# Optimization experiments

Hardware: AMD Instinct MI355X
Metric: run time of the kernel (lower is better)

The kernel has to match this reference:

```python
import jax, jax.numpy as jnp
import numpy as np

B, T, V, NH, HD = 2, 64, 32000, 32, 32  # head_dim == n_head required by the original einsum
C = NH * HD

def setup_inputs() -> dict:
    key = jax.random.key(0)
    k0, k1, k2 = jax.random.split(key, 3)
    return {
        "x": jax.random.normal(k0, (B, T, C), jnp.float32),
        "W_ffn": jax.random.normal(k1, (HD, HD), jnp.float32) / np.sqrt(HD),
        "b_ffn": jnp.zeros((HD,), jnp.float32),
        "temps": jnp.ones((NH,), jnp.float32),
        "vocab_emb": jax.random.normal(k2, (V, C), jnp.float32) * 0.02,
    }

def reference(x, W_ffn, b_ffn, temps, vocab_emb):
    b, t, c = x.shape
    nh = temps.shape[0]
    hd = c // nh
    v = vocab_emb.shape[0]
    # per-head channel FFN: Linear(head_dim, head_dim) with bias -> x @ W^T + b
    xc = x.reshape(b * t, nh, hd)
    ffn = jnp.einsum('bnh,dh->bnd', xc, W_ffn) + b_ffn  # (BT, nh, hd)
    # vocab channels: (nh, V, hd)
    vocab_ch = vocab_emb.reshape(v, nh, hd).transpose(1, 0, 2)
    # Original torch einsum 'bnh,hvd->bnv' contracts ffn's head_dim axis with
    # vocab_ch's n_head axis (equal sizes) AND sums over d. Mathematically this
    # equals contracting against vocab_sum[h, v] = sum_d vocab_ch[h, v, d].
    vocab_sum = vocab_ch.sum(-1)  # (nh==hd, V)
    logits = jnp.einsum('bnh,hv->bnv', ffn, vocab_sum)  # (BT, nh, V)
    temps_c = jnp.clip(temps, 0.1)[None, :, None]
    weights = jax.nn.softmax(logits / temps_c, axis=-1)
    # Original 'bnv,hvd->bnh' likewise sums d: out[b,n,h] = sum_v w[b,n,v]*vocab_sum[h,v]
    out = jnp.einsum('bnv,hv->bnh', weights, vocab_sum)  # (BT, nh, hd)
    return out.reshape(b, t, c)
```

## Files before the change

### kernel.cpp

```cpp
#include <hip/hip_runtime.h>
#include <hip/hip_bf16.h>

#define NV      32000
#define MROWS   4096
#define NSLICE  16
#define PART_STRIDE 1056

typedef __attribute__((ext_vector_type(8))) short short8;
typedef __attribute__((ext_vector_type(16))) float f32x16;
typedef __attribute__((ext_vector_type(4))) float f32x4;

#define OFF_VSB  0
#define OFF_VSTB 2048000
#define OFF_FB   4096000
#define OFF_PART 4358144

#define NVS_BLOCKS 1000
#define NF_BLOCKS  512

static __device__ __forceinline__ unsigned pkbf(float lo, float hi) {
    union { __hip_bfloat162 h; unsigned u; } cv;
    cv.h.x = __float2bfloat16(lo);
    cv.h.y = __float2bfloat16(hi);
    return cv.u;
}
static __device__ __forceinline__ f32x4 ntload(const float* p) {
    return __builtin_nontemporal_load((const f32x4*)p);
}

__global__ __launch_bounds__(256)
void prep_kernel(const float* __restrict__ emb,
                 const float* __restrict__ x, const float* __restrict__ W,
                 const float* __restrict__ bias, const float* __restrict__ temps,
                 unsigned short* __restrict__ vsb,
                 unsigned short* __restrict__ vstb,
                 unsigned short* __restrict__ Fb) {
    const int blk = blockIdx.x;
    const int tid = threadIdx.x;
    if (blk < NVS_BLOCKS) {
        const int vbase = blk * 32;
        const int wave = tid >> 6, lane = tid & 63;
        __shared__ float lds[32][33];
        for (int vl = wave; vl < 32; vl += 4) {
            const float* p = emb + (size_t)(vbase + vl) * 1024 + lane * 4;
            f32x4 a0 = ntload(p), a1 = ntload(p + 256), a2 = ntload(p + 512), a3 = ntload(p + 768);
            float s0 = a0.x + a0.y + a0.z + a0.w;
            float s1 = a1.x + a1.y + a1.z + a1.w;
            float s2 = a2.x + a2.y + a2.z + a2.w;
            float s3 = a3.x + a3.y + a3.z + a3.w;
            s0 += __shfl_xor(s0, 1, 64); s0 += __shfl_xor(s0, 2, 64); s0 += __shfl_xor(s0, 4, 64);
            s1 += __shfl_xor(s1, 1, 64); s1 += __shfl_xor(s1, 2, 64); s1 += __shfl_xor(s1, 4, 64);
            s2 += __shfl_xor(s2, 1, 64); s2 += __shfl_xor(s2, 2, 64); s2 += __shfl_xor(s2, 4, 64);
            s3 += __shfl_xor(s3, 1, 64); s3 += __shfl_xor(s3, 2, 64); s3 += __shfl_xor(s3, 4, 64);
            if ((lane & 7) == 0) {
                int hb = lane >> 3;
                lds[vl][hb]      = s0;
                lds[vl][hb + 8]  = s1;
                lds[vl][hb + 16] = s2;
                lds[vl][hb + 24] = s3;
            }
        }
        __syncthreads();
        {
            int v = tid >> 3, h = (tid & 7) * 4;
            unsigned o[2];
            o[0] = pkbf(lds[v][h],     lds[v][h + 1]);
            o[1] = pkbf(lds[v][h + 2], lds[v][h + 3]);
            *(uint2*)(vsb + (size_t)(vbase + v) * 32 + h) = *(uint2*)o;
        }
        {
            int h = tid >> 3, vi = (tid & 7) * 4;
            unsigned o[2];
            o[0] = pkbf(lds[vi][h],     lds[vi + 1][h]);
            o[1] = pkbf(lds[vi + 2][h], lds[vi + 3][h]);
            *(uint2*)(vstb + (size_t)blk * 1024 + h * 32 + vi) = *(uint2*)o;
        }
    } else {
        int t = (blk - NVS_BLOCKS) * 256 + tid;
        int frow = t >> 5, d = t & 31;
        const float4* xp = (const float4*)(x + (size_t)frow * 32);
        const float4* wp = (const float4*)(W + (size_t)d * 32);
        float s = bias[d];
#pragma unroll
        for (int i = 0; i < 8; ++i) {
            float4 xv = xp[i];
            float4 wv = wp[i];
            s += xv.x * wv.x + xv.y * wv.y + xv.z * wv.z + xv.w * wv.w;
        }
        float sc = 1.44269504088896f / fmaxf(temps[frow & 31], 0.1f);
        __hip_bfloat16 bv = __float2bfloat16(s * sc);
        Fb[t] = *reinterpret_cast<unsigned short*>(&bv);
    }
}

#define TILE(QA, QB, OACC, LSUM) do {                                              \
    f32x16 sa;                                                                     \
    _Pragma("unroll")                                                              \
    for (int r = 0; r < 16; ++r) sa[r] = 0.f;                                      \
    sa = __builtin_amdgcn_mfma_f32_32x32x16_bf16(va0, QA, sa, 0, 0, 0);            \
    sa = __builtin_amdgcn_mfma_f32_32x32x16_bf16(va1, QB, sa, 0, 0, 0);            \
    _Pragma("unroll")                                                              \
    for (int r = 0; r < 16; ++r) sa[r] = __builtin_amdgcn_exp2f(sa[r]);            \
    {                                                                              \
        float t0 = sa[0] + sa[1],   t1 = sa[2] + sa[3];                            \
        float t2 = sa[4] + sa[5],   t3 = sa[6] + sa[7];                            \
        float t4 = sa[8] + sa[9],   t5 = sa[10] + sa[11];                          \
        float t6 = sa[12] + sa[13], t7 = sa[14] + sa[15];                          \
        LSUM += ((t0 + t1) + (t2 + t3)) + ((t4 + t5) + (t6 + t7));                 \
    }                                                                              \
    unsigned u0 = pkbf(sa[0], sa[1]),   u1 = pkbf(sa[2], sa[3]);                   \
    unsigned u2 = pkbf(sa[4], sa[5]),   u3 = pkbf(sa[6], sa[7]);                   \
    unsigned u4 = pkbf(sa[8], sa[9]),   u5 = pkbf(sa[10], sa[11]);                 \
    unsigned u6 = pkbf(sa[12], sa[13]), u7 = pkbf(sa[14], sa[15]);                 \
    asm volatile("v_permlane32_swap_b32 %0, %1" : "+v"(u0), "+v"(u2));             \
    asm volatile("v_permlane32_swap_b32 %0, %1" : "+v"(u1), "+v"(u3));             \
    asm volatile("v_permlane32_swap_b32 %0, %1" : "+v"(u4), "+v"(u6));             \
    asm volatile("v_permlane32_swap_b32 %0, %1" : "+v"(u5), "+v"(u7));             \
    union { unsigned u[4]; short8 v8; } pa0, pa1;                                  \
    pa0.u[0] = u0; pa0.u[1] = u1; pa0.u[2] = u2; pa0.u[3] = u3;                    \
    pa1.u[0] = u4; pa1.u[1] = u5; pa1.u[2] = u6; pa1.u[3] = u7;                    \
    OACC = __builtin_amdgcn_mfma_f32_32x32x16_bf16(pa0.v8, vb0, OACC, 0, 0, 0);    \
    OACC = __builtin_amdgcn_mfma_f32_32x32x16_bf16(pa1.v8, vb1, OACC, 0, 0, 0);    \
} while (0)

__global__ __launch_bounds__(256, 4)
void fused_mfma(const unsigned short* __restrict__ vsb,
                const unsigned short* __restrict__ vstb,
                const unsigned short* __restrict__ Fb,
                float* __restrict__ part) {
    const int b = blockIdx.x;
    const int s = b & 15;
    const int qp = b >> 4;
    const int tid = threadIdx.x;
    const int wave = tid >> 6, lane = tid & 63;
    const int hi = lane >> 5, c = lane & 31;

    const int qrow0 = qp * 64 + c;
    short8 q0a = *(const short8*)(Fb + (size_t)qrow0 * 32 + 8 * hi);
    short8 q0b = *(const short8*)(Fb + (size_t)qrow0 * 32 + 16 + 8 * hi);
    short8 q1a = *(const short8*)(Fb + (size_t)(qrow0 + 32) * 32 + 8 * hi);
    short8 q1b = *(const short8*)(Fb + (size_t)(qrow0 + 32) * 32 + 16 + 8 * hi);

    f32x16 oacc0, oacc1;
#pragma unroll
    for (int r = 0; r < 16; ++r) { oacc0[r] = 0.f; oacc1[r] = 0.f; }
    float lsum0 = 0.f, lsum1 = 0.f;

    const int c1 = (125 * (s + 1)) >> 1;
    const unsigned short* vr_base = vsb + (c << 5) + (hi << 3);
    const unsigned short* vt_base = vstb + (c << 5) + (hi << 3);

    for (int ch = ((125 * s) >> 1) + wave; ch < c1; ch += 4) {
        const unsigned short* vrow = vr_base + ((size_t)ch << 10);
        short8 va0 = *(const short8*)(vrow);
        short8 va1 = *(const short8*)(vrow + 16);
        const unsigned short* vtrow = vt_base + ((size_t)ch << 10);
        short8 vb0 = *(const short8*)(vtrow);
        short8 vb1 = *(const short8*)(vtrow + 16);

        TILE(q0a, q0b, oacc0, lsum0);
        TILE(q1a, q1b, oacc1, lsum1);
    }

    lsum0 += __shfl_xor(lsum0, 32, 64);
    lsum1 += __shfl_xor(lsum1, 32, 64);

    __shared__ float red[2][4][64 * 17];
    __shared__ float lred[2][4][32];
    {
        float* rw0 = &red[0][wave][lane * 17];
        float* rw1 = &red[1][wave][lane * 17];
#pragma unroll
        for (int r = 0; r < 16; ++r) { rw0[r] = oacc0[r]; rw1[r] = oacc1[r]; }
        if (hi == 0) {
            lred[0][wave][c] = lsum0;
            lred[1][wave][c] = lsum1;
        }
    }
    __syncthreads();

#pragma unroll
    for (int t = 0; t < 2; ++t) {
        const size_t pbase = (size_t)((qp * 2 + t) * NSLICE + s) * PART_STRIDE;
        for (int idx = tid; idx < 1024; idx += 256) {
            int ln = idx >> 4, r = idx & 15;
            float sum = red[t][0][ln * 17 + r] + red[t][1][ln * 17 + r]
                      + red[t][2][ln * 17 + r] + red[t][3][ln * 17 + r];
            int lhi = ln >> 5, lc = ln & 31;
            int q = (r & 3) + 8 * (r >> 2) + 4 * lhi;
            part[pbase + (q << 5) + lc] = sum;
        }
        if (tid < 32)
            part[pbase + 1024 + tid] = lred[t][0][tid] + lred[t][1][tid]
                                     + lred[t][2][tid] + lred[t][3][tid];
    }
}

__global__ void combine_kernel(const float* __restrict__ part, float* __restrict__ out) {
    int t = blockIdx.x * 256 + threadIdx.x;
    if (t >= MROWS * 32) return;
    int qrow = t >> 5, j = t & 31;
    int qt = qrow >> 5, qi = qrow & 31;
    float a = 0.f, l = 0.f;
#pragma unroll
    for (int s = 0; s < NSLICE; ++s) {
        const float* p = part + (size_t)(qt * NSLICE + s) * PART_STRIDE;
        a += p[(qi << 5) + j];
        l += p[1024 + qi];
    }
    out[t] = a / l;
}

extern "C" void kernel_launch(void* const* d_in, const int* in_sizes, int n_in,
                              void* d_out, int out_size, void* d_ws, size_t ws_size,
                              hipStream_t stream) {
    const float* x     = (const float*)d_in[0];
    const float* W     = (const float*)d_in[1];
    const float* bias  = (const float*)d_in[2];
    const float* temps = (const float*)d_in[3];
    const float* emb   = (const float*)d_in[4];
    float* out = (float*)d_out;

    char* ws = (char*)d_ws;
    unsigned short* vsb  = (unsigned short*)(ws + OFF_VSB);
    unsigned short* vstb = (unsigned short*)(ws + OFF_VSTB);
    unsigned short* Fb   = (unsigned short*)(ws + OFF_FB);
    float*          part = (float*)(ws + OFF_PART);

    prep_kernel<<<NVS_BLOCKS + NF_BLOCKS, 256, 0, stream>>>(emb, x, W, bias, temps,
                                                            vsb, vstb, Fb);
    fused_mfma<<<64 * NSLICE, 256, 0, stream>>>(vsb, vstb, Fb, part);
    combine_kernel<<<(MROWS * 32 + 255) / 256, 256, 0, stream>>>(part, out);
}
```

Measured before the change: 61.02 us.

## Overlap vocab-sum prep with first half of MFMA slices and fuse combine

Splits the vocab-sum preprocessing into two halves. The first half runs with the F projection in prep1. The second half runs inside a mixed kernel alongside the MFMA slices that only need the first half of the vocabulary. A finish kernel then processes the remaining slices and uses an atomic counter so the last block per query pair performs the final normalization, removing the separate combine launch. This aims to overlap the memory-bound embedding reduction with compute and cut one launch, at the cost of counter atomics, thread fences and some load imbalance in the mixed kernel.

```diff
diff --git a/kernel.cpp b/kernel.cpp
--- a/kernel.cpp
+++ b/kernel.cpp
@@ -14,9 +14,7 @@
 #define OFF_VSTB 2048000
 #define OFF_FB   4096000
 #define OFF_PART 4358144
-
-#define NVS_BLOCKS 1000
-#define NF_BLOCKS  512
+#define OFF_CNT  13008896
 
 static __device__ __forceinline__ unsigned pkbf(float lo, float hi) {
     union { __hip_bfloat162 h; unsigned u; } cv;
@@ -28,69 +26,68 @@
     return __builtin_nontemporal_load((const f32x4*)p);
 }
 
-__global__ __launch_bounds__(256)
-void prep_kernel(const float* __restrict__ emb,
-                 const float* __restrict__ x, const float* __restrict__ W,
-                 const float* __restrict__ bias, const float* __restrict__ temps,
-                 unsigned short* __restrict__ vsb,
-                 unsigned short* __restrict__ vstb,
-                 unsigned short* __restrict__ Fb) {
-    const int blk = blockIdx.x;
-    const int tid = threadIdx.x;
-    if (blk < NVS_BLOCKS) {
-        const int vbase = blk * 32;
-        const int wave = tid >> 6, lane = tid & 63;
-        __shared__ float lds[32][33];
-        for (int vl = wave; vl < 32; vl += 4) {
-            const float* p = emb + (size_t)(vbase + vl) * 1024 + lane * 4;
-            f32x4 a0 = ntload(p), a1 = ntload(p + 256), a2 = ntload(p + 512), a3 = ntload(p + 768);
-            float s0 = a0.x + a0.y + a0.z + a0.w;
-            float s1 = a1.x + a1.y + a1.z + a1.w;
-            float s2 = a2.x + a2.y + a2.z + a2.w;
-            float s3 = a3.x + a3.y + a3.z + a3.w;
-            s0 += __shfl_xor(s0, 1, 64); s0 += __shfl_xor(s0, 2, 64); s0 += __shfl_xor(s0, 4, 64);
-            s1 += __shfl_xor(s1, 1, 64); s1 += __shfl_xor(s1, 2, 64); s1 += __shfl_xor(s1, 4, 64);
-            s2 += __shfl_xor(s2, 1, 64); s2 += __shfl_xor(s2, 2, 64); s2 += __shfl_xor(s2, 4, 64);
-            s3 += __shfl_xor(s3, 1, 64); s3 += __shfl_xor(s3, 2, 64); s3 += __shfl_xor(s3, 4, 64);
-            if ((lane & 7) == 0) {
-                int hb = lane >> 3;
-                lds[vl][hb]      = s0;
-                lds[vl][hb + 8]  = s1;
-                lds[vl][hb + 16] = s2;
-                lds[vl][hb + 24] = s3;
-            }
-        }
-        __syncthreads();
-        {
-            int v = tid >> 3, h = (tid & 7) * 4;
-            unsigned o[2];
-            o[0] = pkbf(lds[v][h],     lds[v][h + 1]);
-            o[1] = pkbf(lds[v][h + 2], lds[v][h + 3]);
-            *(uint2*)(vsb + (size_t)(vbase + v) * 32 + h) = *(uint2*)o;
-        }
-        {
-            int h = tid >> 3, vi = (tid & 7) * 4;
-            unsigned o[2];
-            o[0] = pkbf(lds[vi][h],     lds[vi + 1][h]);
-            o[1] = pkbf(lds[vi + 2][h], lds[vi + 3][h]);
-            *(uint2*)(vstb + (size_t)blk * 1024 + h * 32 + vi) = *(uint2*)o;
-        }
-    } else {
-        int t = (blk - NVS_BLOCKS) * 256 + tid;
-        int frow = t >> 5, d = t & 31;
-        const float4* xp = (const float4*)(x + (size_t)frow * 32);
-        const float4* wp = (const float4*)(W + (size_t)d * 32);
-        float s = bias[d];
-#pragma unroll
-        for (int i = 0; i < 8; ++i) {
-            float4 xv = xp[i];
-            float4 wv = wp[i];
-            s += xv.x * wv.x + xv.y * wv.y + xv.z * wv.z + xv.w * wv.w;
-        }
-        float sc = 1.44269504088896f / fmaxf(temps[frow & 31], 0.1f);
-        __hip_bfloat16 bv = __float2bfloat16(s * sc);
-        Fb[t] = *reinterpret_cast<unsigned short*>(&bv);
-    }
+static __device__ __forceinline__ void prep_chunk(int blk, const float* __restrict__ emb,
+                                                  unsigned short* __restrict__ vsb,
+                                                  unsigned short* __restrict__ vstb,
+                                                  float* __restrict__ smem, int tid) {
+    const int vbase = blk * 32;
+    const int wave = tid >> 6, lane = tid & 63;
+    float (*lds)[33] = (float(*)[33])smem;
+    for (int vl = wave; vl < 32; vl += 4) {
+        const float* p = emb + (size_t)(vbase + vl) * 1024 + lane * 4;
+        f32x4 a0 = ntload(p), a1 = ntload(p + 256), a2 = ntload(p + 512), a3 = ntload(p + 768);
+        float s0 = a0.x + a0.y + a0.z + a0.w;
+        float s1 = a1.x + a1.y + a1.z + a1.w;
+        float s2 = a2.x + a2.y + a2.z + a2.w;
+        float s3 = a3.x + a3.y + a3.z + a3.w;
+        s0 += __shfl_xor(s0, 1, 64); s0 += __shfl_xor(s0, 2, 64); s0 += __shfl_xor(s0, 4, 64);
+        s1 += __shfl_xor(s1, 1, 64); s1 += __shfl_xor(s1, 2, 64); s1 += __shfl_xor(s1, 4, 64);
+        s2 += __shfl_xor(s2, 1, 64); s2 += __shfl_xor(s2, 2, 64); s2 += __shfl_xor(s2, 4, 64);
+        s3 += __shfl_xor(s3, 1, 64); s3 += __shfl_xor(s3, 2, 64); s3 += __shfl_xor(s3, 4, 64);
+        if ((lane & 7) == 0) {
+            int hb = lane >> 3;
+            lds[vl][hb]      = s0;
+            lds[vl][hb + 8]  = s1;
+            lds[vl][hb + 16] = s2;
+            lds[vl][hb + 24] = s3;
+        }
+    }
+    __syncthreads();
+    {
+        int v = tid >> 3, h = (tid & 7) * 4;
+        unsigned o[2];
+        o[0] = pkbf(lds[v][h],     lds[v][h + 1]);
+        o[1] = pkbf(lds[v][h + 2], lds[v][h + 3]);
+        *(uint2*)(vsb + (size_t)(vbase + v) * 32 + h) = *(uint2*)o;
+    }
+    {
+        int h = tid >> 3, vi = (tid & 7) * 4;
+        unsigned o[2];
+        o[0] = pkbf(lds[vi][h],     lds[vi + 1][h]);
+        o[1] = pkbf(lds[vi + 2][h], lds[vi + 3][h]);
+        *(uint2*)(vstb + (size_t)blk * 1024 + h * 32 + vi) = *(uint2*)o;
+    }
+}
+
+static __device__ __forceinline__ void prep_F(int fblk, const float* __restrict__ x,
+                                              const float* __restrict__ W,
+                                              const float* __restrict__ bias,
+                                              const float* __restrict__ temps,
+                                              unsigned short* __restrict__ Fb, int tid) {
+    int t = fblk * 256 + tid;
+    int frow = t >> 5, d = t & 31;
+    const float4* xp = (const float4*)(x + (size_t)frow * 32);
+    const float4* wp = (const float4*)(W + (size_t)d * 32);
+    float s = bias[d];
+#pragma unroll
+    for (int i = 0; i < 8; ++i) {
+        float4 xv = xp[i];
+        float4 wv = wp[i];
+        s += xv.x * wv.x + xv.y * wv.y + xv.z * wv.z + xv.w * wv.w;
+    }
+    float sc = 1.44269504088896f / fmaxf(temps[frow & 31], 0.1f);
+    __hip_bfloat16 bv = __float2bfloat16(s * sc);
+    Fb[t] = *reinterpret_cast<unsigned short*>(&bv);
 }
 
 #define TILE(QA, QB, OACC, LSUM) do {                                              \
@@ -123,15 +120,12 @@
     OACC = __builtin_amdgcn_mfma_f32_32x32x16_bf16(pa1.v8, vb1, OACC, 0, 0, 0);    \
 } while (0)
 
-__global__ __launch_bounds__(256, 4)
-void fused_mfma(const unsigned short* __restrict__ vsb,
-                const unsigned short* __restrict__ vstb,
-                const unsigned short* __restrict__ Fb,
-                float* __restrict__ part) {
-    const int b = blockIdx.x;
-    const int s = b & 15;
-    const int qp = b >> 4;
-    const int tid = threadIdx.x;
+static __device__ __forceinline__ void fused_qs(int qp, int s,
+                                                const unsigned short* __restrict__ vsb,
+                                                const unsigned short* __restrict__ vstb,
+                                                const unsigned short* __restrict__ Fb,
+                                                float* __restrict__ part,
+                                                float* __restrict__ smem, int tid) {
     const int wave = tid >> 6, lane = tid & 63;
     const int hi = lane >> 5, c = lane & 31;
 
@@ -165,16 +159,15 @@
     lsum0 += __shfl_xor(lsum0, 32, 64);
     lsum1 += __shfl_xor(lsum1, 32, 64);
 
-    __shared__ float red[2][4][64 * 17];
-    __shared__ float lred[2][4][32];
+    __syncthreads();
     {
-        float* rw0 = &red[0][wave][lane * 17];
-        float* rw1 = &red[1][wave][lane * 17];
+        float* rw0 = smem + (0 * 4 + wave) * 1088 + lane * 17;
+        float* rw1 = smem + (1 * 4 + wave) * 1088 + lane * 17;
 #pragma unroll
         for (int r = 0; r < 16; ++r) { rw0[r] = oacc0[r]; rw1[r] = oacc1[r]; }
         if (hi == 0) {
-            lred[0][wave][c] = lsum0;
-            lred[1][wave][c] = lsum1;
+            smem[8704 + (0 * 4 + wave) * 32 + c] = lsum0;
+            smem[8704 + (1 * 4 + wave) * 32 + c] = lsum1;
         }
     }
     __syncthreads();
@@ -184,31 +177,81 @@
         const size_t pbase = (size_t)((qp * 2 + t) * NSLICE + s) * PART_STRIDE;
         for (int idx = tid; idx < 1024; idx += 256) {
             int ln = idx >> 4, r = idx & 15;
-            float sum = red[t][0][ln * 17 + r] + red[t][1][ln * 17 + r]
-                      + red[t][2][ln * 17 + r] + red[t][3][ln * 17 + r];
+            float sum = smem[(t * 4 + 0) * 1088 + ln * 17 + r] + smem[(t * 4 + 1) * 1088 + ln * 17 + r]
+                      + smem[(t * 4 + 2) * 1088 + ln * 17 + r] + smem[(t * 4 + 3) * 1088 + ln * 17 + r];
             int lhi = ln >> 5, lc = ln & 31;
             int q = (r & 3) + 8 * (r >> 2) + 4 * lhi;
             part[pbase + (q << 5) + lc] = sum;
         }
         if (tid < 32)
-            part[pbase + 1024 + tid] = lred[t][0][tid] + lred[t][1][tid]
-                                     + lred[t][2][tid] + lred[t][3][tid];
-    }
-}
-
-__global__ void combine_kernel(const float* __restrict__ part, float* __restrict__ out) {
-    int t = blockIdx.x * 256 + threadIdx.x;
-    if (t >= MROWS * 32) return;
-    int qrow = t >> 5, j = t & 31;
-    int qt = qrow >> 5, qi = qrow & 31;
-    float a = 0.f, l = 0.f;
-#pragma unroll
-    for (int s = 0; s < NSLICE; ++s) {
-        const float* p = part + (size_t)(qt * NSLICE + s) * PART_STRIDE;
-        a += p[(qi << 5) + j];
-        l += p[1024 + qi];
-    }
-    out[t] = a / l;
+            part[pbase + 1024 + tid] = smem[8704 + (t * 4 + 0) * 32 + tid] + smem[8704 + (t * 4 + 1) * 32 + tid]
+                                     + smem[8704 + (t * 4 + 2) * 32 + tid] + smem[8704 + (t * 4 + 3) * 32 + tid];
+    }
+}
+
+__global__ __launch_bounds__(256)
+void prep1_kernel(const float* __restrict__ emb, const float* __restrict__ x,
+                  const float* __restrict__ W, const float* __restrict__ bias,
+                  const float* __restrict__ temps,
+                  unsigned short* __restrict__ vsb, unsigned short* __restrict__ vstb,
+                  unsigned short* __restrict__ Fb, int* __restrict__ cnt) {
+    const int b = blockIdx.x;
+    const int tid = threadIdx.x;
+    if (b == 0 && tid < 64) cnt[tid] = 0;
+    __shared__ float smem[32 * 33];
+    if (b < 500) prep_chunk(b, emb, vsb, vstb, smem, tid);
+    else         prep_F(b - 500, x, W, bias, temps, Fb, tid);
+}
+
+__global__ __launch_bounds__(256, 4)
+void mixed_kernel(const float* __restrict__ emb,
+                  const unsigned short* __restrict__ vsb_c, unsigned short* __restrict__ vsb,
+                  const unsigned short* __restrict__ vstb_c, unsigned short* __restrict__ vstb,
+                  const unsigned short* __restrict__ Fb, float* __restrict__ part) {
+    const int b = blockIdx.x;
+    const int tid = threadIdx.x;
+    const int s = b & 15, qp = b >> 4;
+    __shared__ float smem[8960];
+    if (s < 8) {
+        fused_qs(qp, s, vsb_c, vstb_c, Fb, part, smem, tid);
+    } else {
+        int g1 = qp * 8 + (s - 8);
+        if (g1 < 500) prep_chunk(500 + g1, emb, vsb, vstb, smem, tid);
+    }
+}
+
+__global__ __launch_bounds__(256, 4)
+void finish_kernel(const unsigned short* __restrict__ vsb,
+                   const unsigned short* __restrict__ vstb,
+                   const unsigned short* __restrict__ Fb,
+                   float* __restrict__ part, int* __restrict__ cnt,
+                   float* __restrict__ out) {
+    const int b = blockIdx.x;
+    const int tid = threadIdx.x;
+    const int s = 8 + (b & 7), qp = b >> 3;
+    __shared__ float smem[8960];
+    fused_qs(qp, s, vsb, vstb, Fb, part, smem, tid);
+
+    __threadfence();
+    __syncthreads();
+    __shared__ int sdone;
+    if (tid == 0) sdone = (atomicAdd(&cnt[qp], 1) == 7) ? 1 : 0;
+    __syncthreads();
+    if (sdone) {
+        __threadfence();
+        for (int t2 = tid; t2 < 2048; t2 += 256) {
+            int lr = t2 >> 5, j = t2 & 31;
+            int qt = qp * 2 + (lr >> 5), qi = lr & 31;
+            float a = 0.f, l = 0.f;
+#pragma unroll
+            for (int sl = 0; sl < NSLICE; ++sl) {
+                const float* p = part + (size_t)(qt * NSLICE + sl) * PART_STRIDE;
+                a += p[(qi << 5) + j];
+                l += p[1024 + qi];
+            }
+            out[(size_t)qp * 2048 + t2] = a / l;
+        }
+    }
 }
 
 extern "C" void kernel_launch(void* const* d_in, const int* in_sizes, int n_in,
@@ -226,9 +269,9 @@
     unsigned short* vstb = (unsigned short*)(ws + OFF_VSTB);
     unsigned short* Fb   = (unsigned short*)(ws + OFF_FB);
     float*          part = (float*)(ws + OFF_PART);
-
-    prep_kernel<<<NVS_BLOCKS + NF_BLOCKS, 256, 0, stream>>>(emb, x, W, bias, temps,
-                                                            vsb, vstb, Fb);
-    fused_mfma<<<64 * NSLICE, 256, 0, stream>>>(vsb, vstb, Fb, part);
-    combine_kernel<<<(MROWS * 32 + 255) / 256, 256, 0, stream>>>(part, out);
-}
+    int*            cnt  = (int*)(ws + OFF_CNT);
+
+    prep1_kernel<<<1012, 256, 0, stream>>>(emb, x, W, bias, temps, vsb, vstb, Fb, cnt);
+    mixed_kernel<<<1024, 256, 0, stream>>>(emb, vsb, vsb, vstb, vstb, Fb, part);
+    finish_kernel<<<512, 256, 0, stream>>>(vsb, vstb, Fb, part, cnt, out);
+}
```

Measured after the change: 164.3 us. +169.2%, slower.
